# Performance work log

Measured on AMD Instinct MI355X. Metric: run time of the kernel, lower is better.

## Reference

```python
import jax, jax.numpy as jnp
import numpy as np

N = 50000      # nodes
E = 800000     # edges
HID = 128      # hidden_dim (== input_dim)
HEADS = 4
D = HID // HEADS  # 32 head dim
L = 3          # n_layers
G = 64         # graphs in batch
LAT = 64       # latent_dim


def _segment_softmax(logits, seg, num):
    # logits: [E, HEADS], seg: [E] -> softmax over edges sharing the same dst node
    m = jax.ops.segment_max(logits, seg, num_segments=num)          # [N, HEADS]
    e = jnp.exp(logits - m[seg])
    s = jax.ops.segment_sum(e, seg, num_segments=num)               # [N, HEADS]
    return e / (s[seg] + 1e-16)


def setup_inputs() -> dict:
    key = jax.random.key(0)
    ks = jax.random.split(key, 16)
    sc = 0.05
    inp = {
        "x": jax.random.normal(ks[0], (N, HID), dtype=jnp.float32),
        "edge_index": jax.random.randint(ks[1], (2, E), 0, N, dtype=jnp.int32),
        "batch": jnp.sort(jax.random.randint(ks[2], (N,), 0, G, dtype=jnp.int32)),
        # input projection
        "Win": jax.random.normal(ks[3], (HID, HID), dtype=jnp.float32) * sc,
        "bin_": jnp.zeros((HID,), dtype=jnp.float32),
        # per-layer TransformerConv params (stacked over layers)
        "Wq": jax.random.normal(ks[4], (L, HID, HID), dtype=jnp.float32) * sc,
        "bq": jnp.zeros((L, HID), dtype=jnp.float32),
        "Wk": jax.random.normal(ks[5], (L, HID, HID), dtype=jnp.float32) * sc,
        "bk": jnp.zeros((L, HID), dtype=jnp.float32),
        "Wv": jax.random.normal(ks[6], (L, HID, HID), dtype=jnp.float32) * sc,
        "bv": jnp.zeros((L, HID), dtype=jnp.float32),
        "Wskip": jax.random.normal(ks[7], (L, HID, HID), dtype=jnp.float32) * sc,
        "bskip": jnp.zeros((L, HID), dtype=jnp.float32),
        # final fc
        "Wfc": jax.random.normal(ks[8], (LAT, HID), dtype=jnp.float32) * sc,
        "bfc": jnp.zeros((LAT,), dtype=jnp.float32),
    }
    return inp


def reference(x, edge_index, batch, Win, bin_, Wq, bq, Wk, bk, Wv, bv, Wskip, bskip, Wfc, bfc):
    src, dst = edge_index[0], edge_index[1]
    h = x @ Win.T + bin_                                   # [N, HID]
    scale = 1.0 / np.sqrt(D).astype(np.float32)
    for l in range(L):
        q = (h @ Wq[l].T + bq[l]).reshape(N, HEADS, D)
        k = (h @ Wk[l].T + bk[l]).reshape(N, HEADS, D)
        v = (h @ Wv[l].T + bv[l]).reshape(N, HEADS, D)
        # edge-level gather: query at dst, key/value at src
        alpha = jnp.einsum('ehd,ehd->eh', q[dst], k[src]) * scale   # [E, HEADS]
        a = _segment_softmax(alpha, dst, N)                          # [E, HEADS]
        msg = a[..., None] * v[src]                                  # [E, HEADS, D]
        out = jax.ops.segment_sum(msg, dst, num_segments=N).reshape(N, HID)
        h = jax.nn.relu(out + h @ Wskip[l].T + bskip[l])            # root (skip) connection, then ReLU
    pooled = jax.ops.segment_sum(h, batch, num_segments=G)          # global_add_pool -> [G, HID]
    return pooled @ Wfc.T + bfc                                      # [G, LAT]
```

## Files before the change

kernel.cpp:

```cpp
#include <hip/hip_runtime.h>
#include <math.h>

#define NN 50000
#define NE 800000
#define HID 128
#define NL 3
#define NG 64
#define LAT 64

typedef __attribute__((ext_vector_type(8))) short short8v;
typedef __attribute__((ext_vector_type(4))) short short4v;
typedef __attribute__((ext_vector_type(4))) float f32x4;
typedef __attribute__((ext_vector_type(2))) float f32x2;

__device__ __forceinline__ float bf2f(unsigned short b) {
    unsigned u = ((unsigned)b) << 16;
    return __builtin_bit_cast(float, u);
}
__device__ __forceinline__ unsigned short f2bf(float f) {
    unsigned u = __builtin_bit_cast(unsigned, f);
    u += 0x7FFFu + ((u >> 16) & 1u);
    return (unsigned short)(u >> 16);
}

__device__ __forceinline__ float dot8_fp8(int d0, int d1, const float* qf) {
    f32x2 a01 = __builtin_amdgcn_cvt_pk_f32_fp8(d0, false);
    f32x2 a23 = __builtin_amdgcn_cvt_pk_f32_fp8(d0, true);
    f32x2 a45 = __builtin_amdgcn_cvt_pk_f32_fp8(d1, false);
    f32x2 a67 = __builtin_amdgcn_cvt_pk_f32_fp8(d1, true);
    return a01[0]*qf[0] + a01[1]*qf[1] + a23[0]*qf[2] + a23[1]*qf[3]
         + a45[0]*qf[4] + a45[1]*qf[5] + a67[0]*qf[6] + a67[1]*qf[7];
}
__device__ __forceinline__ void acc8_fp8(int d0, int d1, float wgt, float* acc) {
    f32x2 v01 = __builtin_amdgcn_cvt_pk_f32_fp8(d0, false);
    f32x2 v23 = __builtin_amdgcn_cvt_pk_f32_fp8(d0, true);
    f32x2 v45 = __builtin_amdgcn_cvt_pk_f32_fp8(d1, false);
    f32x2 v67 = __builtin_amdgcn_cvt_pk_f32_fp8(d1, true);
    acc[0] += wgt * v01[0]; acc[1] += wgt * v01[1];
    acc[2] += wgt * v23[0]; acc[3] += wgt * v23[1];
    acc[4] += wgt * v45[0]; acc[5] += wgt * v45[1];
    acc[6] += wgt * v67[0]; acc[7] += wgt * v67[1];
}

struct PtrTab { const float* p[13]; };

__global__ __launch_bounds__(256) void pack_all_kernel(
    PtrTab wt, PtrTab bt, short* __restrict__ Wcat, float* __restrict__ bcat,
    int* __restrict__ deg, float* __restrict__ pooled)
{
    int gid = blockIdx.x * 256 + threadIdx.x;
    if (gid < 13 * 16384) {
        int slot = gid >> 14, e = gid & 16383;
        Wcat[gid] = (short)f2bf(wt.p[slot][e]);
    }
    if (gid < 13 * 128) {
        int slot = gid >> 7, e = gid & 127;
        bcat[gid] = bt.p[slot][e];
    }
    if (gid < NN) deg[gid] = 0;
    if (gid < NG * HID) pooled[gid] = 0.f;
}

template<int NM, int CVT>
__global__ __launch_bounds__((NM == 4) ? 512 : 256, 2) void gemm_mfma(
    const void* __restrict__ Av, const short* __restrict__ Wcat,
    const float* __restrict__ bias, short* __restrict__ out,
    signed char* __restrict__ kv8, int nrows)
{
    constexpr int NC  = NM * 128;
    constexpr int KST = (NM == 4) ? 2 : 1;
    constexpr int KBS = 16 / KST;
    constexpr int WN  = (NM == 4) ? 4 : 1;
    constexpr int WM  = (NM == 4) ? 2 : 4;
    constexpr int NTH = WN * WM * 64;
    constexpr int CH  = KBS * NC / NTH;
    constexpr int CSTR = NC + 4;
    constexpr int QROWS = WM * 16;
    constexpr int CHK = QROWS * (NC / 8) / NTH;
    constexpr int SMEM_W = KBS * NC * 8 * 2;
    constexpr int SMEM_C = QROWS * CSTR * 2;
    constexpr int SMEM = (SMEM_W > SMEM_C) ? SMEM_W : SMEM_C;
    __shared__ char smem[SMEM];
    short* Wlds = (short*)smem;
    short* Clds = (short*)smem;

    const short* Ab = (const short*)Av;
    const float* Af = (const float*)Av;

    const int tid  = threadIdx.x;
    const int lane = tid & 63;
    const int wid  = tid >> 6;
    const int wn = wid % WN;
    const int wm = wid / WN;
    const int blockbase = blockIdx.x * (WM * 64);
    const int rbase = blockbase + wm * 64;
    const int r0 = rbase + (lane & 15);
    const int n0 = wn * 128;
    const int lg = lane >> 4;

    f32x4 acc[4][8];
#pragma unroll
    for (int i = 0; i < 4; ++i)
#pragma unroll
        for (int j = 0; j < 8; ++j) acc[i][j] = {0.f, 0.f, 0.f, 0.f};

    const short8v zero8 = {0, 0, 0, 0, 0, 0, 0, 0};
    short8v wreg[CH];

    auto stage_load = [&](int st) {
#pragma unroll
        for (int c2 = 0; c2 < CH; ++c2) {
            int c = tid + NTH * c2;
            int j = c & (NC - 1);
            int kb = st * KBS + c / NC;
            wreg[c2] = *reinterpret_cast<const short8v*>(&Wcat[j * HID + kb * 8]);
        }
    };
    auto stage_write = [&]() {
#pragma unroll
        for (int c2 = 0; c2 < CH; ++c2) {
            int c = tid + NTH * c2;
            int j = c & (NC - 1);
            int kbl = c / NC;
            *reinterpret_cast<short8v*>(&Wlds[(kbl * NC + j) * 8]) = wreg[c2];
        }
    };
    auto compute_stage = [&](int s_lo, int s_hi) {
        for (int s = s_lo; s < s_hi; ++s) {
            short8v a[4], b[8];
#pragma unroll
            for (int mf = 0; mf < 4; ++mf) {
                int row = r0 + mf * 16;
                if (CVT) {
                    if (row < nrows) {
                        const float* ap = Af + (size_t)row * HID + s * 32 + lg * 8;
                        float4 f0 = *reinterpret_cast<const float4*>(ap);
                        float4 f1 = *reinterpret_cast<const float4*>(ap + 4);
                        short8v t;
                        t[0] = (short)f2bf(f0.x); t[1] = (short)f2bf(f0.y);
                        t[2] = (short)f2bf(f0.z); t[3] = (short)f2bf(f0.w);
                        t[4] = (short)f2bf(f1.x); t[5] = (short)f2bf(f1.y);
                        t[6] = (short)f2bf(f1.z); t[7] = (short)f2bf(f1.w);
                        a[mf] = t;
                    } else a[mf] = zero8;
                } else {
                    a[mf] = (row < nrows)
                        ? *reinterpret_cast<const short8v*>(&Ab[(size_t)row * HID + s * 32 + lg * 8])
                        : zero8;
                }
            }
            const int kbl = (s - s_lo) * 4 + lg;
#pragma unroll
            for (int nf = 0; nf < 8; ++nf) {
                int slot = kbl * NC + n0 + nf * 16 + (lane & 15);
                b[nf] = *reinterpret_cast<const short8v*>(&Wlds[slot * 8]);
            }
#pragma unroll
            for (int mf = 0; mf < 4; ++mf)
#pragma unroll
                for (int nf = 0; nf < 8; ++nf)
                    acc[mf][nf] = __builtin_amdgcn_mfma_f32_16x16x32_bf16(
                        a[mf], b[nf], acc[mf][nf], 0, 0, 0);
        }
    };

    stage_load(0);
    stage_write();
    if (KST == 2) stage_load(1);
    __syncthreads();
    compute_stage(0, 4 / KST);
    if (KST == 2) {
        __syncthreads();
        stage_write();
        __syncthreads();
        compute_stage(2, 4);
    }

#pragma unroll
    for (int mf = 0; mf < 4; ++mf) {
        __syncthreads();
#pragma unroll
        for (int nf = 0; nf < 8; ++nf) {
            int col = n0 + nf * 16 + (lane & 15);
            float bv = bias[col];
#pragma unroll
            for (int qq = 0; qq < 4; ++qq) {
                int rl = wm * 16 + lg * 4 + qq;
                Clds[rl * CSTR + col] = (short)f2bf(acc[mf][nf][qq] + bv);
            }
        }
        __syncthreads();
#pragma unroll
        for (int i = 0; i < CHK; ++i) {
            int c = tid + NTH * i;
            int rl = c / (NC / 8);
            int ck = c % (NC / 8);
            int grow = blockbase + (rl >> 4) * 64 + mf * 16 + (rl & 15);
            if (grow < nrows) {
                if (NM == 1) {
                    *reinterpret_cast<short8v*>(&out[(size_t)grow * NC + ck * 8]) =
                        *reinterpret_cast<const short8v*>(&Clds[rl * CSTR + ck * 8]);
                } else if (ck < 16) {
                    *reinterpret_cast<short8v*>(&out[(size_t)grow * 256 + ck * 8]) =
                        *reinterpret_cast<const short8v*>(&Clds[rl * CSTR + ck * 8]);
                } else if (ck < 48) {
                    short8v cv = *reinterpret_cast<const short8v*>(&Clds[rl * CSTR + ck * 8]);
                    float f0 = bf2f((unsigned short)cv[0]), f1 = bf2f((unsigned short)cv[1]);
                    float f2 = bf2f((unsigned short)cv[2]), f3 = bf2f((unsigned short)cv[3]);
                    float f4 = bf2f((unsigned short)cv[4]), f5 = bf2f((unsigned short)cv[5]);
                    float f6 = bf2f((unsigned short)cv[6]), f7 = bf2f((unsigned short)cv[7]);
                    int w0 = __builtin_amdgcn_cvt_pk_fp8_f32(f0, f1, 0, false);
                    w0     = __builtin_amdgcn_cvt_pk_fp8_f32(f2, f3, w0, true);
                    int w1 = __builtin_amdgcn_cvt_pk_fp8_f32(f4, f5, 0, false);
                    w1     = __builtin_amdgcn_cvt_pk_fp8_f32(f6, f7, w1, true);
                    int off = (ck < 32) ? (ck - 16) * 16 : ((ck - 32) * 16 + 8);
                    *reinterpret_cast<int2*>(kv8 + (size_t)grow * 256 + off) =
                        make_int2(w0, w1);
                } else {
                    *reinterpret_cast<short8v*>(&out[(size_t)grow * 256 + 128 + (ck - 48) * 8]) =
                        *reinterpret_cast<const short8v*>(&Clds[rl * CSTR + ck * 8]);
                }
            }
        }
    }
}

__global__ __launch_bounds__(256) void count_deg_kernel(
    const int* __restrict__ dst, int* __restrict__ deg,
    unsigned short* __restrict__ rank16, int ne)
{
    int e = blockIdx.x * 256 + threadIdx.x;
    if (e < ne) {
        int r = atomicAdd(&deg[dst[e]], 1);
        rank16[e] = (unsigned short)r;
    }
}

__global__ __launch_bounds__(1024) void scan1_kernel(
    const int* __restrict__ deg, int* __restrict__ offsets,
    int* __restrict__ bsum, int n)
{
    __shared__ int wsum[16];
    const int tid = threadIdx.x, wid = tid >> 6, lane = tid & 63;
    int i = blockIdx.x * 1024 + tid;
    int val = (i < n) ? deg[i] : 0;
    int x = val;
#pragma unroll
    for (int off = 1; off < 64; off <<= 1) {
        int y = __shfl_up(x, off);
        if (lane >= off) x += y;
    }
    if (lane == 63) wsum[wid] = x;
    __syncthreads();
    if (tid < 16) {
        int w = wsum[tid];
#pragma unroll
        for (int off = 1; off < 16; off <<= 1) {
            int y = __shfl_up(w, off);
            if (tid >= off) w += y;
        }
        wsum[tid] = w;
    }
    __syncthreads();
    int incl = x + (wid ? wsum[wid - 1] : 0);
    if (i < n) offsets[i + 1] = incl;
    if (tid == 1023) bsum[blockIdx.x] = incl;
}

__global__ __launch_bounds__(256) void scan3_kernel(
    int* __restrict__ offsets, const int* __restrict__ bsum, int n, int nb)
{
    __shared__ int sx[64];
    const int tid = threadIdx.x;
    if (tid < 64) {
        int vv = (tid < nb) ? bsum[tid] : 0;
        int x = vv;
#pragma unroll
        for (int off = 1; off < 64; off <<= 1) {
            int y = __shfl_up(x, off);
            if (tid >= off) x += y;
        }
        sx[tid] = x - vv;
    }
    __syncthreads();
    int i = blockIdx.x * 256 + tid;
    if (i >= n) return;
    offsets[i + 1] += sx[i >> 10];
    if (i == 0) offsets[0] = 0;
}

__global__ __launch_bounds__(256) void scatter_kernel(
    const int* __restrict__ src, const int* __restrict__ dst,
    const int* __restrict__ offsets, const unsigned short* __restrict__ rank16,
    unsigned short* __restrict__ csr16, int ne)
{
    int e = blockIdx.x * 256 + threadIdx.x;
    if (e < ne) {
        int pos = offsets[dst[e]] + rank16[e];
        csr16[pos] = (unsigned short)src[e];
    }
}

__global__ __launch_bounds__(256) void attn_kernel(
    const short* __restrict__ qs, const signed char* __restrict__ kv8,
    const int* __restrict__ offsets, const unsigned short* __restrict__ csr16,
    short* __restrict__ hout, int nnodes)
{
    int node = (blockIdx.x * 256 + threadIdx.x) >> 6;
    if (node >= nnodes) return;
    const int lane = threadIdx.x & 63;
    const int grp = lane >> 4;
    const int g   = lane & 15;
    const float scale = 0.17677669529663687f;

    const size_t nb = (size_t)node * 256;
    short8v q8 = *reinterpret_cast<const short8v*>(&qs[nb + g * 8]);
    float qf[8];
#pragma unroll
    for (int i = 0; i < 8; ++i) qf[i] = bf2f((unsigned short)q8[i]);

    int e0 = offsets[node], e1 = offsets[node + 1];
    float s = 0.f;
    float acc[8] = {0.f, 0.f, 0.f, 0.f, 0.f, 0.f, 0.f, 0.f};

    const signed char* kvb = kv8 + g * 16;

    int e = e0 + grp;
    int i0 = (e < e1)     ? (int)csr16[e]     : 0;
    int i1 = (e + 4 < e1) ? (int)csr16[e + 4] : 0;

    for (; e + 4 < e1; e += 8) {
        int j0 = (e + 8  < e1) ? (int)csr16[e + 8]  : 0;
        int j1 = (e + 12 < e1) ? (int)csr16[e + 12] : 0;
        int4 kv0 = *reinterpret_cast<const int4*>(kvb + ((size_t)i0 << 8));
        int4 kv1 = *reinterpret_cast<const int4*>(kvb + ((size_t)i1 << 8));
        float p0 = dot8_fp8(kv0.x, kv0.y, qf);
        float p1 = dot8_fp8(kv1.x, kv1.y, qf);
        p0 += __shfl_xor(p0, 1);  p1 += __shfl_xor(p1, 1);
        p0 += __shfl_xor(p0, 2);  p1 += __shfl_xor(p1, 2);
        float w0 = __expf(fminf(p0 * scale, 60.f));
        float w1 = __expf(fminf(p1 * scale, 60.f));
        s += w0 + w1;
        acc8_fp8(kv0.z, kv0.w, w0, acc);
        acc8_fp8(kv1.z, kv1.w, w1, acc);
        i0 = j0; i1 = j1;
    }
    if (e < e1) {
        int4 kv0 = *reinterpret_cast<const int4*>(kvb + ((size_t)i0 << 8));
        float p0 = dot8_fp8(kv0.x, kv0.y, qf);
        p0 += __shfl_xor(p0, 1);
        p0 += __shfl_xor(p0, 2);
        float w0 = __expf(fminf(p0 * scale, 60.f));
        s += w0;
        acc8_fp8(kv0.z, kv0.w, w0, acc);
    }

#pragma unroll
    for (int off = 16; off <= 32; off <<= 1) {
        s += __shfl_xor(s, off);
#pragma unroll
        for (int i = 0; i < 8; ++i) acc[i] += __shfl_xor(acc[i], off);
    }
    float inv = 1.f / (s + 1e-16f);
    short8v sk8 = *reinterpret_cast<const short8v*>(&qs[nb + 128 + g * 8]);
    short8v o;
#pragma unroll
    for (int i = 0; i < 8; ++i) {
        float ov = fmaxf(acc[i] * inv + bf2f((unsigned short)sk8[i]), 0.f);
        o[i] = (short)f2bf(ov);
    }
    *reinterpret_cast<short8v*>(&hout[(size_t)node * HID + g * 8]) = o;
}

__global__ __launch_bounds__(256) void pool_kernel(
    const short* __restrict__ h, const int* __restrict__ batch,
    float* __restrict__ pooled, int nnodes)
{
    const int ROWS = 256;
    int n0 = blockIdx.x * ROWS;
    if (n0 >= nnodes) return;
    int n1 = min(n0 + ROWS, nnodes);
    int rg = threadIdx.x >> 5;
    int c4 = threadIdx.x & 31;
    float s0 = 0.f, s1 = 0.f, s2 = 0.f, s3 = 0.f;
    int g = -1;
    for (int n = n0 + rg; n < n1; n += 8) {
        int bg = batch[n];
        if (bg != g) {
            if (g >= 0) {
                atomicAdd(&pooled[g * HID + c4 * 4 + 0], s0);
                atomicAdd(&pooled[g * HID + c4 * 4 + 1], s1);
                atomicAdd(&pooled[g * HID + c4 * 4 + 2], s2);
                atomicAdd(&pooled[g * HID + c4 * 4 + 3], s3);
            }
            s0 = s1 = s2 = s3 = 0.f;
            g = bg;
        }
        short4v hv = *reinterpret_cast<const short4v*>(&h[(size_t)n * HID + c4 * 4]);
        s0 += bf2f((unsigned short)hv[0]);
        s1 += bf2f((unsigned short)hv[1]);
        s2 += bf2f((unsigned short)hv[2]);
        s3 += bf2f((unsigned short)hv[3]);
    }
    if (g >= 0) {
        atomicAdd(&pooled[g * HID + c4 * 4 + 0], s0);
        atomicAdd(&pooled[g * HID + c4 * 4 + 1], s1);
        atomicAdd(&pooled[g * HID + c4 * 4 + 2], s2);
        atomicAdd(&pooled[g * HID + c4 * 4 + 3], s3);
    }
}

__global__ __launch_bounds__(256) void fc_kernel(
    const float* __restrict__ pooled, const float* __restrict__ Wfc,
    const float* __restrict__ bfc, float* __restrict__ out)
{
    int t = blockIdx.x * 256 + threadIdx.x;
    if (t >= NG * LAT) return;
    int g = t >> 6, o = t & 63;
    float sum = bfc[o];
    for (int j = 0; j < HID; ++j)
        sum += pooled[g * HID + j] * Wfc[o * HID + j];
    out[t] = sum;
}

extern "C" void kernel_launch(void* const* d_in, const int* in_sizes, int n_in,
                              void* d_out, int out_size, void* d_ws, size_t ws_size,
                              hipStream_t stream)
{
    const float* x     = (const float*)d_in[0];
    const int*   ei    = (const int*)d_in[1];
    const int*   batch = (const int*)d_in[2];
    const float* Win   = (const float*)d_in[3];
    const float* bin_  = (const float*)d_in[4];
    const float* Wq    = (const float*)d_in[5];
    const float* bq    = (const float*)d_in[6];
    const float* Wk    = (const float*)d_in[7];
    const float* bk    = (const float*)d_in[8];
    const float* Wv    = (const float*)d_in[9];
    const float* bv    = (const float*)d_in[10];
    const float* Wskip = (const float*)d_in[11];
    const float* bskip = (const float*)d_in[12];
    const float* Wfc   = (const float*)d_in[13];
    const float* bfc   = (const float*)d_in[14];
    float* out = (float*)d_out;

    char* ws = (char*)d_ws;
    auto alloc = [&](size_t bytes) {
        void* p = (void*)ws;
        ws += (bytes + 255) & ~(size_t)255;
        return p;
    };
    short* hb     = (short*)alloc((size_t)NN * HID * 2);
    short* qs     = (short*)alloc((size_t)NN * 256 * 2);
    signed char* kv8 = (signed char*)alloc((size_t)NN * 256);
    short* Wcat   = (short*)alloc((size_t)13 * 16384 * 2);
    float* bcat   = (float*)alloc((size_t)13 * 128 * 4);
    float* pooled = (float*)alloc((size_t)NG * HID * 4);
    int* deg      = (int*)alloc((size_t)NN * 4);
    int* offsets  = (int*)alloc((size_t)(NN + 1) * 4);
    int* bsum     = (int*)alloc((size_t)64 * 4);
    unsigned short* rank16 = (unsigned short*)alloc((size_t)NE * 2);
    unsigned short* csr16  = (unsigned short*)alloc((size_t)NE * 2);

    const int* esrc = ei;
    const int* edst = ei + NE;

    PtrTab wt, bt;
    wt.p[0] = Win; bt.p[0] = bin_;
    for (int l = 0; l < NL; ++l) {
        wt.p[1 + 4 * l] = Wq    + (size_t)l * HID * HID;
        wt.p[2 + 4 * l] = Wk    + (size_t)l * HID * HID;
        wt.p[3 + 4 * l] = Wv    + (size_t)l * HID * HID;
        wt.p[4 + 4 * l] = Wskip + (size_t)l * HID * HID;
        bt.p[1 + 4 * l] = bq    + (size_t)l * HID;
        bt.p[2 + 4 * l] = bk    + (size_t)l * HID;
        bt.p[3 + 4 * l] = bv    + (size_t)l * HID;
        bt.p[4 + 4 * l] = bskip + (size_t)l * HID;
    }

    pack_all_kernel<<<(13 * 16384) / 256, 256, 0, stream>>>(wt, bt, Wcat, bcat, deg, pooled);

    const int egrid = (NE + 255) / 256;
    const int nsb = (NN + 1023) / 1024;
    count_deg_kernel<<<egrid, 256, 0, stream>>>(edst, deg, rank16, NE);
    scan1_kernel<<<nsb, 1024, 0, stream>>>(deg, offsets, bsum, NN);
    scan3_kernel<<<(NN + 255) / 256, 256, 0, stream>>>(offsets, bsum, NN, nsb);
    scatter_kernel<<<egrid, 256, 0, stream>>>(esrc, edst, offsets, rank16, csr16, NE);

    gemm_mfma<1, 1><<<(NN + 255) / 256, 256, 0, stream>>>(
        x, Wcat, bcat, hb, (signed char*)nullptr, NN);

    const int g4 = (NN + 127) / 128;
    for (int l = 0; l < NL; ++l) {
        gemm_mfma<4, 0><<<g4, 512, 0, stream>>>(
            hb, Wcat + (size_t)(1 + 4 * l) * 16384, bcat + (1 + 4 * l) * 128, qs, kv8, NN);
        attn_kernel<<<(NN + 3) / 4, 256, 0, stream>>>(qs, kv8, offsets, csr16, hb, NN);
    }

    pool_kernel<<<(NN + 255) / 256, 256, 0, stream>>>(hb, batch, pooled, NN);
    fc_kernel<<<16, 256, 0, stream>>>(pooled, Wfc, bfc, out);
}
```

Baseline: 310.7 us.

## Pre-transpose layer weights into MFMA-ready layout and read B directly from global

```diff
diff --git a/kernel.cpp b/kernel.cpp
--- a/kernel.cpp
+++ b/kernel.cpp
@@ -45,13 +45,21 @@
 struct PtrTab { const float* p[13]; };
 
 __global__ __launch_bounds__(256) void pack_all_kernel(
-    PtrTab wt, PtrTab bt, short* __restrict__ Wcat, float* __restrict__ bcat,
-    int* __restrict__ deg, float* __restrict__ pooled)
+    PtrTab wt, PtrTab bt, short* __restrict__ Wcat, short* __restrict__ Wt,
+    float* __restrict__ bcat, int* __restrict__ deg, float* __restrict__ pooled)
 {
     int gid = blockIdx.x * 256 + threadIdx.x;
-    if (gid < 13 * 16384) {
-        int slot = gid >> 14, e = gid & 16383;
-        Wcat[gid] = (short)f2bf(wt.p[slot][e]);
+    if (gid < 16384) {
+        Wcat[gid] = (short)f2bf(wt.p[0][gid]);
+    }
+    if (gid < 12 * 16384) {
+        int i  = gid & 7;
+        int c  = (gid >> 3) & 511;
+        int kb = (gid >> 12) & 15;
+        int l  = gid >> 16;
+        int slot = 1 + 4 * l + (c >> 7);
+        int elem = (c & 127) * 128 + kb * 8 + i;
+        Wt[gid] = (short)f2bf(wt.p[slot][elem]);
     }
     if (gid < 13 * 128) {
         int slot = gid >> 7, e = gid & 127;
@@ -61,147 +69,78 @@
     if (gid < NG * HID) pooled[gid] = 0.f;
 }
 
-template<int NM, int CVT>
-__global__ __launch_bounds__((NM == 4) ? 512 : 256, 2) void gemm_mfma(
-    const void* __restrict__ Av, const short* __restrict__ Wcat,
-    const float* __restrict__ bias, short* __restrict__ out,
+__global__ __launch_bounds__(512) void gemm_layer(
+    const short* __restrict__ A, const short* __restrict__ Wt_l,
+    const float* __restrict__ bias, short* __restrict__ qs,
     signed char* __restrict__ kv8, int nrows)
 {
-    constexpr int NC  = NM * 128;
-    constexpr int KST = (NM == 4) ? 2 : 1;
-    constexpr int KBS = 16 / KST;
-    constexpr int WN  = (NM == 4) ? 4 : 1;
-    constexpr int WM  = (NM == 4) ? 2 : 4;
-    constexpr int NTH = WN * WM * 64;
-    constexpr int CH  = KBS * NC / NTH;
-    constexpr int CSTR = NC + 4;
-    constexpr int QROWS = WM * 16;
-    constexpr int CHK = QROWS * (NC / 8) / NTH;
-    constexpr int SMEM_W = KBS * NC * 8 * 2;
-    constexpr int SMEM_C = QROWS * CSTR * 2;
-    constexpr int SMEM = (SMEM_W > SMEM_C) ? SMEM_W : SMEM_C;
-    __shared__ char smem[SMEM];
-    short* Wlds = (short*)smem;
-    short* Clds = (short*)smem;
-
-    const short* Ab = (const short*)Av;
-    const float* Af = (const float*)Av;
+    constexpr int CSTR = 516;
+    __shared__ short Clds[16 * CSTR];
 
     const int tid  = threadIdx.x;
     const int lane = tid & 63;
     const int wid  = tid >> 6;
-    const int wn = wid % WN;
-    const int wm = wid / WN;
-    const int blockbase = blockIdx.x * (WM * 64);
-    const int rbase = blockbase + wm * 64;
-    const int r0 = rbase + (lane & 15);
-    const int n0 = wn * 128;
-    const int lg = lane >> 4;
-
-    f32x4 acc[4][8];
+    const int n0   = wid * 64;
+    const int lg   = lane >> 4;
+    const int l15  = lane & 15;
+    const int rb   = blockIdx.x * 64;
+    const int r0   = rb + l15;
+
+    f32x4 acc[4][4];
 #pragma unroll
     for (int i = 0; i < 4; ++i)
 #pragma unroll
-        for (int j = 0; j < 8; ++j) acc[i][j] = {0.f, 0.f, 0.f, 0.f};
+        for (int j = 0; j < 4; ++j) acc[i][j] = {0.f, 0.f, 0.f, 0.f};
 
     const short8v zero8 = {0, 0, 0, 0, 0, 0, 0, 0};
-    short8v wreg[CH];
-
-    auto stage_load = [&](int st) {
-#pragma unroll
-        for (int c2 = 0; c2 < CH; ++c2) {
-            int c = tid + NTH * c2;
-            int j = c & (NC - 1);
-            int kb = st * KBS + c / NC;
-            wreg[c2] = *reinterpret_cast<const short8v*>(&Wcat[j * HID + kb * 8]);
-        }
-    };
-    auto stage_write = [&]() {
-#pragma unroll
-        for (int c2 = 0; c2 < CH; ++c2) {
-            int c = tid + NTH * c2;
-            int j = c & (NC - 1);
-            int kbl = c / NC;
-            *reinterpret_cast<short8v*>(&Wlds[(kbl * NC + j) * 8]) = wreg[c2];
-        }
-    };
-    auto compute_stage = [&](int s_lo, int s_hi) {
-        for (int s = s_lo; s < s_hi; ++s) {
-            short8v a[4], b[8];
-#pragma unroll
-            for (int mf = 0; mf < 4; ++mf) {
-                int row = r0 + mf * 16;
-                if (CVT) {
-                    if (row < nrows) {
-                        const float* ap = Af + (size_t)row * HID + s * 32 + lg * 8;
-                        float4 f0 = *reinterpret_cast<const float4*>(ap);
-                        float4 f1 = *reinterpret_cast<const float4*>(ap + 4);
-                        short8v t;
-                        t[0] = (short)f2bf(f0.x); t[1] = (short)f2bf(f0.y);
-                        t[2] = (short)f2bf(f0.z); t[3] = (short)f2bf(f0.w);
-                        t[4] = (short)f2bf(f1.x); t[5] = (short)f2bf(f1.y);
-                        t[6] = (short)f2bf(f1.z); t[7] = (short)f2bf(f1.w);
-                        a[mf] = t;
-                    } else a[mf] = zero8;
-                } else {
-                    a[mf] = (row < nrows)
-                        ? *reinterpret_cast<const short8v*>(&Ab[(size_t)row * HID + s * 32 + lg * 8])
-                        : zero8;
-                }
-            }
-            const int kbl = (s - s_lo) * 4 + lg;
-#pragma unroll
-            for (int nf = 0; nf < 8; ++nf) {
-                int slot = kbl * NC + n0 + nf * 16 + (lane & 15);
-                b[nf] = *reinterpret_cast<const short8v*>(&Wlds[slot * 8]);
-            }
-#pragma unroll
-            for (int mf = 0; mf < 4; ++mf)
-#pragma unroll
-                for (int nf = 0; nf < 8; ++nf)
-                    acc[mf][nf] = __builtin_amdgcn_mfma_f32_16x16x32_bf16(
-                        a[mf], b[nf], acc[mf][nf], 0, 0, 0);
-        }
-    };
-
-    stage_load(0);
-    stage_write();
-    if (KST == 2) stage_load(1);
-    __syncthreads();
-    compute_stage(0, 4 / KST);
-    if (KST == 2) {
-        __syncthreads();
-        stage_write();
-        __syncthreads();
-        compute_stage(2, 4);
+
+#pragma unroll
+    for (int s = 0; s < 4; ++s) {
+        short8v a[4], b[4];
+#pragma unroll
+        for (int mf = 0; mf < 4; ++mf) {
+            int row = r0 + mf * 16;
+            a[mf] = (row < nrows)
+                ? *reinterpret_cast<const short8v*>(&A[(size_t)row * HID + s * 32 + lg * 8])
+                : zero8;
+        }
+        const int kb = s * 4 + lg;
+#pragma unroll
+        for (int nf = 0; nf < 4; ++nf) {
+            int col = n0 + nf * 16 + l15;
+            b[nf] = *reinterpret_cast<const short8v*>(&Wt_l[((size_t)kb * 512 + col) * 8]);
+        }
+#pragma unroll
+        for (int mf = 0; mf < 4; ++mf)
+#pragma unroll
+            for (int nf = 0; nf < 4; ++nf)
+                acc[mf][nf] = __builtin_amdgcn_mfma_f32_16x16x32_bf16(
+                    a[mf], b[nf], acc[mf][nf], 0, 0, 0);
     }
 
 #pragma unroll
     for (int mf = 0; mf < 4; ++mf) {
         __syncthreads();
 #pragma unroll
-        for (int nf = 0; nf < 8; ++nf) {
-            int col = n0 + nf * 16 + (lane & 15);
+        for (int nf = 0; nf < 4; ++nf) {
+            int col = n0 + nf * 16 + l15;
             float bv = bias[col];
 #pragma unroll
             for (int qq = 0; qq < 4; ++qq) {
-                int rl = wm * 16 + lg * 4 + qq;
+                int rl = lg * 4 + qq;
                 Clds[rl * CSTR + col] = (short)f2bf(acc[mf][nf][qq] + bv);
             }
         }
         __syncthreads();
 #pragma unroll
-        for (int i = 0; i < CHK; ++i) {
-            int c = tid + NTH * i;
-            int rl = c / (NC / 8);
-            int ck = c % (NC / 8);
-            int grow = blockbase + (rl >> 4) * 64 + mf * 16 + (rl & 15);
+        for (int i = 0; i < 2; ++i) {
+            int c = tid + 512 * i;
+            int rl = c >> 6;
+            int ck = c & 63;
+            int grow = rb + mf * 16 + rl;
             if (grow < nrows) {
-                if (NM == 1) {
-                    *reinterpret_cast<short8v*>(&out[(size_t)grow * NC + ck * 8]) =
-                        *reinterpret_cast<const short8v*>(&Clds[rl * CSTR + ck * 8]);
-                } else if (ck < 16) {
-                    *reinterpret_cast<short8v*>(&out[(size_t)grow * 256 + ck * 8]) =
+                if (ck < 16) {
+                    *reinterpret_cast<short8v*>(&qs[(size_t)grow * 256 + ck * 8]) =
                         *reinterpret_cast<const short8v*>(&Clds[rl * CSTR + ck * 8]);
                 } else if (ck < 48) {
                     short8v cv = *reinterpret_cast<const short8v*>(&Clds[rl * CSTR + ck * 8]);
@@ -217,10 +156,102 @@
                     *reinterpret_cast<int2*>(kv8 + (size_t)grow * 256 + off) =
                         make_int2(w0, w1);
                 } else {
-                    *reinterpret_cast<short8v*>(&out[(size_t)grow * 256 + 128 + (ck - 48) * 8]) =
+                    *reinterpret_cast<short8v*>(&qs[(size_t)grow * 256 + 128 + (ck - 48) * 8]) =
                         *reinterpret_cast<const short8v*>(&Clds[rl * CSTR + ck * 8]);
                 }
             }
+        }
+    }
+}
+
+__global__ __launch_bounds__(256, 2) void gemm_in(
+    const float* __restrict__ Af, const short* __restrict__ Wcat,
+    const float* __restrict__ bias, short* __restrict__ out, int nrows)
+{
+    constexpr int CSTR = 132;
+    __shared__ short smem[16 * 128 * 8];
+    short* Wlds = smem;
+    short* Clds = smem;
+
+    const int tid  = threadIdx.x;
+    const int lane = tid & 63;
+    const int wid  = tid >> 6;
+    const int blockbase = blockIdx.x * 256;
+    const int rbase = blockbase + wid * 64;
+    const int r0 = rbase + (lane & 15);
+    const int lg = lane >> 4;
+
+    for (int c = tid; c < 128 * 16; c += 256) {
+        int j = c & 127;
+        int kb = c >> 7;
+        *reinterpret_cast<short8v*>(&Wlds[(kb * 128 + j) * 8]) =
+            *reinterpret_cast<const short8v*>(&Wcat[j * HID + kb * 8]);
+    }
+    __syncthreads();
+
+    f32x4 acc[4][8];
+#pragma unroll
+    for (int i = 0; i < 4; ++i)
+#pragma unroll
+        for (int j = 0; j < 8; ++j) acc[i][j] = {0.f, 0.f, 0.f, 0.f};
+
+    const short8v zero8 = {0, 0, 0, 0, 0, 0, 0, 0};
+    for (int s = 0; s < 4; ++s) {
+        short8v a[4], b[8];
+#pragma unroll
+        for (int mf = 0; mf < 4; ++mf) {
+            int row = r0 + mf * 16;
+            if (row < nrows) {
+                const float* ap = Af + (size_t)row * HID + s * 32 + lg * 8;
+                float4 f0 = *reinterpret_cast<const float4*>(ap);
+                float4 f1 = *reinterpret_cast<const float4*>(ap + 4);
+                short8v t;
+                t[0] = (short)f2bf(f0.x); t[1] = (short)f2bf(f0.y);
+                t[2] = (short)f2bf(f0.z); t[3] = (short)f2bf(f0.w);
+                t[4] = (short)f2bf(f1.x); t[5] = (short)f2bf(f1.y);
+                t[6] = (short)f2bf(f1.z); t[7] = (short)f2bf(f1.w);
+                a[mf] = t;
+            } else a[mf] = zero8;
+        }
+        const int kb = s * 4 + lg;
+#pragma unroll
+        for (int nf = 0; nf < 8; ++nf) {
+            int slot = kb * 128 + nf * 16 + (lane & 15);
+            b[nf] = *reinterpret_cast<const short8v*>(&Wlds[slot * 8]);
+        }
+#pragma unroll
+        for (int mf = 0; mf < 4; ++mf)
+#pragma unroll
+            for (int nf = 0; nf < 8; ++nf)
+                acc[mf][nf] = __builtin_amdgcn_mfma_f32_16x16x32_bf16(
+                    a[mf], b[nf], acc[mf][nf], 0, 0, 0);
+    }
+
+#pragma unroll
+    for (int mf = 0; mf < 4; ++mf) {
+        __syncthreads();
+#pragma unroll
+        for (int nf = 0; nf < 8; ++nf) {
+            int col = nf * 16 + (lane & 15);
+            float bv = bias[col];
+#pragma unroll
+            for (int qq = 0; qq < 4; ++qq) {
+                int rl = wid * 4 + lg;
+                (void)rl;
+                Clds[(wid * 16 + lg * 4 + qq) * CSTR + col] =
+                    (short)f2bf(acc[mf][nf][qq] + bv);
+            }
+        }
+        __syncthreads();
+#pragma unroll
+        for (int i = 0; i < 4; ++i) {
+            int c = tid + 256 * i;
+            int rl = c >> 4;
+            int ck = c & 15;
+            int grow = blockbase + (rl >> 4) * 64 + mf * 16 + (rl & 15);
+            if (grow < nrows)
+                *reinterpret_cast<short8v*>(&out[(size_t)grow * HID + ck * 8]) =
+                    *reinterpret_cast<const short8v*>(&Clds[rl * CSTR + ck * 8]);
         }
     }
 }
@@ -453,7 +484,8 @@
     short* hb     = (short*)alloc((size_t)NN * HID * 2);
     short* qs     = (short*)alloc((size_t)NN * 256 * 2);
     signed char* kv8 = (signed char*)alloc((size_t)NN * 256);
-    short* Wcat   = (short*)alloc((size_t)13 * 16384 * 2);
+    short* Wcat   = (short*)alloc((size_t)16384 * 2);
+    short* Wt     = (short*)alloc((size_t)12 * 16384 * 2);
     float* bcat   = (float*)alloc((size_t)13 * 128 * 4);
     float* pooled = (float*)alloc((size_t)NG * HID * 4);
     int* deg      = (int*)alloc((size_t)NN * 4);
@@ -478,7 +510,8 @@
         bt.p[4 + 4 * l] = bskip + (size_t)l * HID;
     }
 
-    pack_all_kernel<<<(13 * 16384) / 256, 256, 0, stream>>>(wt, bt, Wcat, bcat, deg, pooled);
+    pack_all_kernel<<<(12 * 16384 + 255) / 256, 256, 0, stream>>>(
+        wt, bt, Wcat, Wt, bcat, deg, pooled);
 
     const int egrid = (NE + 255) / 256;
     const int nsb = (NN + 1023) / 1024;
@@ -487,13 +520,12 @@
     scan3_kernel<<<(NN + 255) / 256, 256, 0, stream>>>(offsets, bsum, NN, nsb);
     scatter_kernel<<<egrid, 256, 0, stream>>>(esrc, edst, offsets, rank16, csr16, NE);
 
-    gemm_mfma<1, 1><<<(NN + 255) / 256, 256, 0, stream>>>(
-        x, Wcat, bcat, hb, (signed char*)nullptr, NN);
-
-    const int g4 = (NN + 127) / 128;
+    gemm_in<<<(NN + 255) / 256, 256, 0, stream>>>(x, Wcat, bcat, hb, NN);
+
+    const int gl = (NN + 63) / 64;
     for (int l = 0; l < NL; ++l) {
-        gemm_mfma<4, 0><<<g4, 512, 0, stream>>>(
-            hb, Wcat + (size_t)(1 + 4 * l) * 16384, bcat + (1 + 4 * l) * 128, qs, kv8, NN);
+        gemm_layer<<<gl, 512, 0, stream>>>(
+            hb, Wt + (size_t)l * 16 * 512 * 8, bcat + (1 + 4 * l) * 128, qs, kv8, NN);
         attn_kernel<<<(NN + 3) / 4, 256, 0, stream>>>(qs, kv8, offsets, csr16, hb, NN);
     }
 
```

Result: faster. 295.0 us (-5.1%).
